# Kernel tuning notes

Measured on AMD Instinct MI355X. Metric: run time of the kernel, lower is better.

## Reference

```python
import jax, jax.numpy as jnp
import numpy as np
import math

B, C, H, W = 32, 256, 64, 64
AUX, RANK, HID, OS = 64, 64, 256, 8


def _fourier(u):
    # u: [B, r] -> take first r//2, sin/cos with freqs linspace(1, pi)
    half = RANK // 2
    w = jnp.linspace(1.0, math.pi, half, dtype=u.dtype)[None, :]
    u = u[:, :half]
    return jnp.concatenate([jnp.sin(u * w), jnp.cos(u * w)], axis=-1)


def setup_inputs() -> dict:
    key = jax.random.key(0)
    ks = jax.random.split(key, 10)

    def lin(k, fan_in, fan_out):
        k1, k2 = jax.random.split(k)
        Wm = jax.random.normal(k1, (fan_in, fan_out), jnp.float32) * 0.02
        bv = jax.random.normal(k2, (fan_out,), jnp.float32) * 0.02
        return Wm, bv

    d = C + AUX
    W_pre, b_pre = lin(ks[0], d, HID)
    W_bc, b_bc = lin(ks[1], HID, C)
    W_bs, b_bs = lin(ks[2], HID, OS)
    W_pc, b_pc = lin(ks[3], HID, RANK)
    W_ps, b_ps = lin(ks[4], HID, RANK)
    W_Wc, b_Wc = lin(ks[5], HID, C * RANK)
    W_Ws, b_Ws = lin(ks[6], HID, OS * RANK)
    x = jax.random.normal(ks[7], (B, C, H, W), jnp.float32)
    a = jax.random.normal(ks[8], (B, AUX), jnp.float32)
    return dict(x=x, a=a, W_pre=W_pre, b_pre=b_pre, W_bc=W_bc, b_bc=b_bc,
                W_bs=W_bs, b_bs=b_bs, W_pc=W_pc, b_pc=b_pc, W_ps=W_ps,
                b_ps=b_ps, W_Wc=W_Wc, b_Wc=b_Wc, W_Ws=W_Ws, b_Ws=b_Ws)


def _m2dm(x, a, W_pre, b_pre, W_bc, b_bc, W_bs, b_bs, W_pc, b_pc,
          W_ps, b_ps, W_Wc, b_Wc, W_Ws, b_Ws):
    Bn, Cn, Hn, Wn = x.shape
    # DynamicProjection
    g = x.mean(axis=(2, 3))                                    # [B,C] GAP
    h = jax.nn.relu(jnp.concatenate([g, a], axis=-1) @ W_pre + b_pre)
    m_base_c = h @ W_bc + b_bc                                 # [B,C]
    m_base_s = h @ W_bs + b_bs                                 # [B,8]
    phi_c = _fourier(h @ W_pc + b_pc)                          # [B,r]
    phi_s = _fourier(h @ W_ps + b_ps)                          # [B,r]
    Wc = (h @ W_Wc + b_Wc).reshape(Bn, Cn, RANK)
    Ws = (h @ W_Ws + b_Ws).reshape(Bn, OS, RANK)
    c_m = m_base_c * jnp.einsum('bcr,br->bc', Wc, phi_c)
    s_m = m_base_s * jnp.einsum('bsr,br->bs', Ws, phi_s)

    # channel modulation
    xc = x * jax.nn.sigmoid(c_m)[:, :, None, None]

    # SpatialModulation: per-sample cross-shaped 3x3 stencil on [avg,max]
    av = x.mean(axis=1)
    mx = x.max(axis=1)
    y = jnp.stack([av, mx], axis=1)                            # [B,2,H,W]
    p = s_m[:, :8].reshape(Bn, 2, 4)                           # up,down,left,right

    def shift(z, di, dj):
        # s[h,w] = z[h+di, w+dj] with zero padding (matches conv2d padding=1)
        zp = jnp.pad(z, ((0, 0), (0, 0), (1, 1), (1, 1)))
        return zp[:, :, 1 + di:1 + di + Hn, 1 + dj:1 + dj + Wn]

    up = shift(y, -1, 0)   # k[0,1] pairs with input row h-1
    dn = shift(y, 1, 0)    # k[2,1]
    lf = shift(y, 0, -1)   # k[1,0]
    rt = shift(y, 0, 1)    # k[1,2]
    pw = p[..., None, None]                                    # [B,2,4,1,1]
    center = -p.sum(axis=-1)[..., None, None]                  # k[1,1] = -sum
    conv = (pw[:, :, 0] * up + pw[:, :, 1] * dn +
            pw[:, :, 2] * lf + pw[:, :, 3] * rt + center * y).sum(axis=1)  # [B,H,W]
    xs = x * jax.nn.sigmoid(conv)[:, None, :, :]
    return x + xc + xs


def reference(x, a, W_pre, b_pre, W_bc, b_bc, W_bs, b_bs, W_pc, b_pc,
              W_ps, b_ps, W_Wc, b_Wc, W_Ws, b_Ws):
    return _m2dm(x, a, W_pre, b_pre, W_bc, b_bc, W_bs, b_bs, W_pc, b_pc,
                 W_ps, b_ps, W_Wc, b_Wc, W_Ws, b_Ws)
```

## Files before the change

### kernel.cpp

```cpp
#include <hip/hip_runtime.h>
#include <math.h>

#define BN   32
#define CN   256
#define HWN  4096
#define AUXN 64
#define RANKN 64
#define HIDN 256
#define OSN  8

#define WS_GPART 0
#define WS_H     131072
#define WS_PHIC  139264
#define WS_MBC   141312
#define WS_SM    149504
#define WS_SIGC  149760
#define WS_Y     157952
#define WS_SIGS  420096

#define TSTR 264

__global__ __launch_bounds__(256) void k_stats(const float* __restrict__ x,
                                               float* __restrict__ gpart,
                                               float* __restrict__ y) {
  int b = blockIdx.y, tile = blockIdx.x, t = threadIdx.x;
  int px = tile * 256 + t;
  const float* xb = x + (size_t)b * CN * HWN;
  __shared__ __align__(16) float tl[64 * TSTR];
  __shared__ float red[256];
  float s = 0.f, m = -INFINITY;
  float* gp = gpart + ((size_t)b * 16 + tile) * 256;
  for (int cc = 0; cc < 4; cc++) {
#pragma unroll 16
    for (int cl = 0; cl < 64; cl++) {
      float v = xb[(size_t)(cc * 64 + cl) * HWN + px];
      s += v;
      m = fmaxf(m, v);
      tl[cl * TSTR + t] = v;
    }
    __syncthreads();
    {
      int cl = t >> 2, pg = t & 3;
      const float4* row = (const float4*)(tl + cl * TSTR + pg * 64);
      float4 acc = {0.f, 0.f, 0.f, 0.f};
#pragma unroll
      for (int j = 0; j < 16; j++) {
        float4 v4 = row[j];
        acc.x += v4.x; acc.y += v4.y; acc.z += v4.z; acc.w += v4.w;
      }
      red[t] = acc.x + acc.y + acc.z + acc.w;
    }
    __syncthreads();
    if (t < 64) gp[cc * 64 + t] = red[t * 4] + red[t * 4 + 1] + red[t * 4 + 2] + red[t * 4 + 3];
    __syncthreads();
  }
  y[(size_t)(b * 2 + 0) * HWN + px] = s * (1.0f / 256.0f);
  y[(size_t)(b * 2 + 1) * HWN + px] = m;
}

__global__ __launch_bounds__(256) void k_head(
    const float* __restrict__ gpart, const float* __restrict__ a,
    const float* __restrict__ W_pre, const float* __restrict__ b_pre,
    const float* __restrict__ W_bc,  const float* __restrict__ b_bc,
    const float* __restrict__ W_bs,  const float* __restrict__ b_bs,
    const float* __restrict__ W_pc,  const float* __restrict__ b_pc,
    const float* __restrict__ W_ps,  const float* __restrict__ b_ps,
    const float* __restrict__ W_Ws,  const float* __restrict__ b_Ws,
    float* __restrict__ h_out, float* __restrict__ phic_out,
    float* __restrict__ mbc_out, float* __restrict__ sm_out) {
  int b = blockIdx.x, t = threadIdx.x;
  __shared__ float in_s[320];
  __shared__ float h_s[256];
  __shared__ float phic_s[64], phis_s[64];
  __shared__ float red[512];
  {
    float gsum = 0.f;
#pragma unroll
    for (int tile = 0; tile < 16; tile++) gsum += gpart[((size_t)b * 16 + tile) * 256 + t];
    in_s[t] = gsum * (1.0f / 4096.0f);
  }
  if (t < 64) in_s[256 + t] = a[b * 64 + t];
  __syncthreads();
  float acc = b_pre[t];
  for (int k = 0; k < 320; k++) acc = fmaf(in_s[k], W_pre[k * 256 + t], acc);
  float h = fmaxf(acc, 0.f);
  h_s[t] = h;
  h_out[b * 256 + t] = h;
  __syncthreads();
  if (t < 64) {
    int j = t & 31;
    const float* Wp = (t < 32) ? W_pc : W_ps;
    const float* bp = (t < 32) ? b_pc : b_ps;
    float u = bp[j];
    for (int k = 0; k < 256; k++) u = fmaf(h_s[k], Wp[k * 64 + j], u);
    float wj = 1.0f + (float)j * (3.14159265358979323846f - 1.0f) / 31.0f;
    float su = sinf(u * wj), cu = cosf(u * wj);
    float* ph = (t < 32) ? phic_s : phis_s;
    ph[j] = su;
    ph[32 + j] = cu;
  }
  __syncthreads();
  if (t < 64) phic_out[b * 64 + t] = phic_s[t];
  float mb = b_bc[t];
  for (int k = 0; k < 256; k++) mb = fmaf(h_s[k], W_bc[k * 256 + t], mb);
  mbc_out[b * 256 + t] = mb;
#pragma unroll
  for (int i = 0; i < 2; i++) {
    int idx = t + 256 * i;
    int s = idx >> 6, r = idx & 63;
    float v = b_Ws[s * 64 + r];
    for (int k = 0; k < 256; k++) v = fmaf(h_s[k], W_Ws[k * 512 + s * 64 + r], v);
    red[idx] = v * phis_s[r];
  }
  __syncthreads();
  if (t < 8) {
    float mbs = b_bs[t];
    for (int k = 0; k < 256; k++) mbs = fmaf(h_s[k], W_bs[k * 8 + t], mbs);
    float sum = 0.f;
    for (int r = 0; r < 64; r++) sum += red[t * 64 + r];
    sm_out[b * 8 + t] = mbs * sum;
  }
}

__global__ __launch_bounds__(512) void k_cm_conv(
    const float* __restrict__ W_Wc, const float* __restrict__ b_Wc,
    const float* __restrict__ h_ws, const float* __restrict__ phic_ws,
    const float* __restrict__ mbc_ws, float* __restrict__ sigc_out,
    const float* __restrict__ y, const float* __restrict__ sm,
    float* __restrict__ sigs) {
  __shared__ __align__(16) float smem[27136];
  int t = threadIdx.x;
  if (blockIdx.x < 256) {
    int c = blockIdx.x;
    float* wsl   = smem;
    float* h_s   = smem + 16384;
    float* phi_s = smem + 24576;
    float* red   = smem + 26624;
    const float* col = W_Wc + (size_t)c * 64;
    for (int i = t; i < 16384; i += 512) {
      int k = i >> 6, r = i & 63;
      wsl[i] = col[(size_t)k * 16384 + r];
    }
    for (int i = t; i < 8192; i += 512) {
      int b = i >> 8, k = i & 255;
      h_s[k * 32 + b] = h_ws[i];
    }
    for (int i = t; i < 2048; i += 512) phi_s[i] = phic_ws[i];
    __syncthreads();
    int b = t >> 4, rq = t & 15;
    float4 q = {0.f, 0.f, 0.f, 0.f};
    const float4* wv = (const float4*)wsl;
    for (int k = 0; k < 256; k++) {
      float4 w4 = wv[k * 16 + rq];
      float hb = h_s[k * 32 + b];
      q.x = fmaf(hb, w4.x, q.x);
      q.y = fmaf(hb, w4.y, q.y);
      q.z = fmaf(hb, w4.z, q.z);
      q.w = fmaf(hb, w4.w, q.w);
    }
    int r0 = rq * 4;
    float4 bw = ((const float4*)(b_Wc + (size_t)c * 64))[rq];
    float part = (q.x + bw.x) * phi_s[b * 64 + r0 + 0] +
                 (q.y + bw.y) * phi_s[b * 64 + r0 + 1] +
                 (q.z + bw.z) * phi_s[b * 64 + r0 + 2] +
                 (q.w + bw.w) * phi_s[b * 64 + r0 + 3];
    red[t] = part;
    __syncthreads();
    if (t < 32) {
      float sum = 0.f;
      for (int i = 0; i < 16; i++) sum += red[t * 16 + i];
      float v = mbc_ws[t * 256 + c] * sum;
      sigc_out[t * 256 + c] = 1.f / (1.f + expf(-v));
    }
  } else {
    int b = blockIdx.x - 256;
    float* ys = smem;
    float* pc = smem + 8192;
    for (int i = t; i < 8192; i += 512) ys[i] = y[b * 8192 + i];
    if (t < 8) pc[t] = sm[b * 8 + t];
    __syncthreads();
    if (t == 0) {
      pc[8] = -(pc[0] + pc[1] + pc[2] + pc[3]);
      pc[9] = -(pc[4] + pc[5] + pc[6] + pc[7]);
    }
    __syncthreads();
    for (int px = t; px < 4096; px += 512) {
      int i = px >> 6, j = px & 63;
      float conv = 0.f;
#pragma unroll
      for (int k = 0; k < 2; k++) {
        const float* yk = ys + k * 4096;
        float up = (i > 0)  ? yk[px - 64] : 0.f;
        float dn = (i < 63) ? yk[px + 64] : 0.f;
        float lf = (j > 0)  ? yk[px - 1]  : 0.f;
        float rt = (j < 63) ? yk[px + 1]  : 0.f;
        conv += pc[k * 4 + 0] * up + pc[k * 4 + 1] * dn + pc[k * 4 + 2] * lf +
                pc[k * 4 + 3] * rt + pc[8 + k] * yk[px];
      }
      sigs[b * 4096 + px] = 1.f / (1.f + expf(-conv));
    }
  }
}

__global__ __launch_bounds__(256) void k_final(const float* __restrict__ x,
                                               const float* __restrict__ sigc,
                                               const float* __restrict__ sigs,
                                               float* __restrict__ out) {
  size_t idx4 = (size_t)blockIdx.x * 256 + threadIdx.x;
  size_t flat = idx4 * 4;
  int b = (int)(flat >> 20);
  int c = (int)((flat >> 12) & 255);
  int px = (int)(flat & 4095);
  float4 xv = ((const float4*)x)[idx4];
  float sc = 1.0f + sigc[b * 256 + c];
  float4 ss = ((const float4*)sigs)[((size_t)b * HWN + px) >> 2];
  float4 o;
  o.x = xv.x * (sc + ss.x);
  o.y = xv.y * (sc + ss.y);
  o.z = xv.z * (sc + ss.z);
  o.w = xv.w * (sc + ss.w);
  ((float4*)out)[idx4] = o;
}

extern "C" void kernel_launch(void* const* d_in, const int* in_sizes, int n_in,
                              void* d_out, int out_size, void* d_ws, size_t ws_size,
                              hipStream_t stream) {
  const float* x     = (const float*)d_in[0];
  const float* a     = (const float*)d_in[1];
  const float* W_pre = (const float*)d_in[2];
  const float* b_pre = (const float*)d_in[3];
  const float* W_bc  = (const float*)d_in[4];
  const float* b_bc  = (const float*)d_in[5];
  const float* W_bs  = (const float*)d_in[6];
  const float* b_bs  = (const float*)d_in[7];
  const float* W_pc  = (const float*)d_in[8];
  const float* b_pc  = (const float*)d_in[9];
  const float* W_ps  = (const float*)d_in[10];
  const float* b_ps  = (const float*)d_in[11];
  const float* W_Wc  = (const float*)d_in[12];
  const float* b_Wc  = (const float*)d_in[13];
  const float* W_Ws  = (const float*)d_in[14];
  const float* b_Ws  = (const float*)d_in[15];
  float* out = (float*)d_out;
  float* ws  = (float*)d_ws;

  float* gpart_ws = ws + WS_GPART;
  float* h_ws     = ws + WS_H;
  float* phic_ws  = ws + WS_PHIC;
  float* mbc_ws   = ws + WS_MBC;
  float* sm_ws    = ws + WS_SM;
  float* sigc_ws  = ws + WS_SIGC;
  float* y_ws     = ws + WS_Y;
  float* sigs_ws  = ws + WS_SIGS;

  k_stats<<<dim3(16, BN), 256, 0, stream>>>(x, gpart_ws, y_ws);
  k_head<<<BN, 256, 0, stream>>>(gpart_ws, a, W_pre, b_pre, W_bc, b_bc, W_bs, b_bs,
                                 W_pc, b_pc, W_ps, b_ps, W_Ws, b_Ws,
                                 h_ws, phic_ws, mbc_ws, sm_ws);
  k_cm_conv<<<CN + BN, 512, 0, stream>>>(W_Wc, b_Wc, h_ws, phic_ws, mbc_ws, sigc_ws,
                                         y_ws, sm_ws, sigs_ws);
  k_final<<<(BN * CN * HWN) / 4 / 256, 256, 0, stream>>>(x, sigc_ws, sigs_ws, out);
}
```

Baseline: 364.5 us.

## Restructure stats reduction, move spatial conv into head, retile channel-modulation GEMV

k_stats now reads x as float4 with each wave covering 64 channels, builds per-channel partial sums through a padded LDS tile, and merges the sum/max across waves. The spatial conv moves from k_cm_conv into k_head, and h is stored transposed so k_cm can copy it with vectorised loads. k_cm is retiled so each thread covers 8 batches with K split across 8 groups and a two-stage reduction, reusing each loaded weight vector 8 times. The head also splits the phi and base-s projections over more threads. The goal is fewer memory passes and better data reuse, at the cost of more LDS use and extra reduction steps.

```diff
diff --git a/kernel.cpp b/kernel.cpp
--- a/kernel.cpp
+++ b/kernel.cpp
@@ -10,7 +10,7 @@
 #define OSN  8
 
 #define WS_GPART 0
-#define WS_H     131072
+#define WS_HT    131072
 #define WS_PHIC  139264
 #define WS_MBC   141312
 #define WS_SM    149504
@@ -18,44 +18,56 @@
 #define WS_Y     157952
 #define WS_SIGS  420096
 
-#define TSTR 264
-
 __global__ __launch_bounds__(256) void k_stats(const float* __restrict__ x,
                                                float* __restrict__ gpart,
                                                float* __restrict__ y) {
   int b = blockIdx.y, tile = blockIdx.x, t = threadIdx.x;
-  int px = tile * 256 + t;
-  const float* xb = x + (size_t)b * CN * HWN;
-  __shared__ __align__(16) float tl[64 * TSTR];
-  __shared__ float red[256];
-  float s = 0.f, m = -INFINITY;
-  float* gp = gpart + ((size_t)b * 16 + tile) * 256;
-  for (int cc = 0; cc < 4; cc++) {
-#pragma unroll 16
-    for (int cl = 0; cl < 64; cl++) {
-      float v = xb[(size_t)(cc * 64 + cl) * HWN + px];
-      s += v;
-      m = fmaxf(m, v);
-      tl[cl * TSTR + t] = v;
+  int w = t >> 6, l = t & 63;
+  __shared__ float csum[256 * 65];
+  __shared__ float4 s_comb[4][64];
+  __shared__ float4 m_comb[4][64];
+  const float4* xb4 = (const float4*)(x + (size_t)b * CN * HWN + tile * 256);
+  float4 s4 = {0.f, 0.f, 0.f, 0.f};
+  float4 m4 = {-INFINITY, -INFINITY, -INFINITY, -INFINITY};
+  int c0 = w << 6;
+#pragma unroll 8
+  for (int cl = 0; cl < 64; cl++) {
+    int c = c0 + cl;
+    float4 v = xb4[(size_t)c * 1024 + l];
+    s4.x += v.x; s4.y += v.y; s4.z += v.z; s4.w += v.w;
+    m4.x = fmaxf(m4.x, v.x); m4.y = fmaxf(m4.y, v.y);
+    m4.z = fmaxf(m4.z, v.z); m4.w = fmaxf(m4.w, v.w);
+    csum[c * 65 + l] = (v.x + v.y) + (v.z + v.w);
+  }
+  s_comb[w][l] = s4;
+  m_comb[w][l] = m4;
+  __syncthreads();
+  {
+    const volatile float* row = csum + t * 65;
+    float g0 = 0.f, g1 = 0.f, g2 = 0.f, g3 = 0.f;
+#pragma unroll
+    for (int j = 0; j < 64; j += 4) {
+      g0 += row[j]; g1 += row[j + 1]; g2 += row[j + 2]; g3 += row[j + 3];
     }
-    __syncthreads();
-    {
-      int cl = t >> 2, pg = t & 3;
-      const float4* row = (const float4*)(tl + cl * TSTR + pg * 64);
-      float4 acc = {0.f, 0.f, 0.f, 0.f};
-#pragma unroll
-      for (int j = 0; j < 16; j++) {
-        float4 v4 = row[j];
-        acc.x += v4.x; acc.y += v4.y; acc.z += v4.z; acc.w += v4.w;
-      }
-      red[t] = acc.x + acc.y + acc.z + acc.w;
-    }
-    __syncthreads();
-    if (t < 64) gp[cc * 64 + t] = red[t * 4] + red[t * 4 + 1] + red[t * 4 + 2] + red[t * 4 + 3];
-    __syncthreads();
-  }
-  y[(size_t)(b * 2 + 0) * HWN + px] = s * (1.0f / 256.0f);
-  y[(size_t)(b * 2 + 1) * HWN + px] = m;
+    gpart[(((size_t)b * 16 + tile) << 8) + t] = (g0 + g1) + (g2 + g3);
+  }
+  if (w == 0) {
+    float4 a0 = s_comb[0][l], a1 = s_comb[1][l], a2 = s_comb[2][l], a3 = s_comb[3][l];
+    float4 b0 = m_comb[0][l], b1 = m_comb[1][l], b2 = m_comb[2][l], b3 = m_comb[3][l];
+    float4 sa, ma;
+    sa.x = (a0.x + a1.x) + (a2.x + a3.x);
+    sa.y = (a0.y + a1.y) + (a2.y + a3.y);
+    sa.z = (a0.z + a1.z) + (a2.z + a3.z);
+    sa.w = (a0.w + a1.w) + (a2.w + a3.w);
+    ma.x = fmaxf(fmaxf(b0.x, b1.x), fmaxf(b2.x, b3.x));
+    ma.y = fmaxf(fmaxf(b0.y, b1.y), fmaxf(b2.y, b3.y));
+    ma.z = fmaxf(fmaxf(b0.z, b1.z), fmaxf(b2.z, b3.z));
+    ma.w = fmaxf(fmaxf(b0.w, b1.w), fmaxf(b2.w, b3.w));
+    const float inv = 1.0f / 256.0f;
+    float4 avg = {sa.x * inv, sa.y * inv, sa.z * inv, sa.w * inv};
+    ((float4*)(y + (size_t)b * 2 * HWN + tile * 256))[l] = avg;
+    ((float4*)(y + ((size_t)b * 2 + 1) * HWN + tile * 256))[l] = ma;
+  }
 }
 
 __global__ __launch_bounds__(256) void k_head(
@@ -66,17 +78,21 @@
     const float* __restrict__ W_pc,  const float* __restrict__ b_pc,
     const float* __restrict__ W_ps,  const float* __restrict__ b_ps,
     const float* __restrict__ W_Ws,  const float* __restrict__ b_Ws,
-    float* __restrict__ h_out, float* __restrict__ phic_out,
-    float* __restrict__ mbc_out, float* __restrict__ sm_out) {
+    const float* __restrict__ y,
+    float* __restrict__ h_t_out, float* __restrict__ phic_out,
+    float* __restrict__ mbc_out, float* __restrict__ sigs) {
   int b = blockIdx.x, t = threadIdx.x;
   __shared__ float in_s[320];
   __shared__ float h_s[256];
   __shared__ float phic_s[64], phis_s[64];
   __shared__ float red[512];
+  __shared__ float red2[256];
+  __shared__ float pc[10];
   {
     float gsum = 0.f;
 #pragma unroll
-    for (int tile = 0; tile < 16; tile++) gsum += gpart[((size_t)b * 16 + tile) * 256 + t];
+    for (int tile = 0; tile < 16; tile++)
+      gsum += gpart[(((size_t)b * 16 + tile) << 8) + t];
     in_s[t] = gsum * (1.0f / 4096.0f);
   }
   if (t < 64) in_s[256 + t] = a[b * 64 + t];
@@ -85,14 +101,21 @@
   for (int k = 0; k < 320; k++) acc = fmaf(in_s[k], W_pre[k * 256 + t], acc);
   float h = fmaxf(acc, 0.f);
   h_s[t] = h;
-  h_out[b * 256 + t] = h;
+  h_t_out[t * 32 + b] = h;
+  __syncthreads();
+  {
+    int ui = t & 63, kg = t >> 6, j = ui & 31;
+    const float* Wp = (ui < 32) ? W_pc : W_ps;
+    float u = 0.f;
+    int k0 = kg << 6;
+    for (int k = k0; k < k0 + 64; k++) u = fmaf(h_s[k], Wp[k * 64 + j], u);
+    red2[(ui << 2) | kg] = u;
+  }
   __syncthreads();
   if (t < 64) {
     int j = t & 31;
-    const float* Wp = (t < 32) ? W_pc : W_ps;
     const float* bp = (t < 32) ? b_pc : b_ps;
-    float u = bp[j];
-    for (int k = 0; k < 256; k++) u = fmaf(h_s[k], Wp[k * 64 + j], u);
+    float u = bp[j] + (red2[t * 4] + red2[t * 4 + 1]) + (red2[t * 4 + 2] + red2[t * 4 + 3]);
     float wj = 1.0f + (float)j * (3.14159265358979323846f - 1.0f) / 31.0f;
     float su = sinf(u * wj), cu = cosf(u * wj);
     float* ph = (t < 32) ? phic_s : phis_s;
@@ -112,93 +135,118 @@
     for (int k = 0; k < 256; k++) v = fmaf(h_s[k], W_Ws[k * 512 + s * 64 + r], v);
     red[idx] = v * phis_s[r];
   }
+  {
+    int s = t & 7, kg = t >> 3;
+    float v = 0.f;
+    int k0 = kg << 3;
+#pragma unroll
+    for (int k = k0; k < k0 + 8; k++) v = fmaf(h_s[k], W_bs[k * 8 + s], v);
+    red2[t] = v;
+  }
   __syncthreads();
   if (t < 8) {
     float mbs = b_bs[t];
-    for (int k = 0; k < 256; k++) mbs = fmaf(h_s[k], W_bs[k * 8 + t], mbs);
+#pragma unroll
+    for (int kg = 0; kg < 32; kg++) mbs += red2[kg * 8 + t];
     float sum = 0.f;
     for (int r = 0; r < 64; r++) sum += red[t * 64 + r];
-    sm_out[b * 8 + t] = mbs * sum;
-  }
-}
-
-__global__ __launch_bounds__(512) void k_cm_conv(
+    pc[t] = mbs * sum;
+  }
+  __syncthreads();
+  if (t == 0) {
+    pc[8] = -(pc[0] + pc[1] + pc[2] + pc[3]);
+    pc[9] = -(pc[4] + pc[5] + pc[6] + pc[7]);
+  }
+  __syncthreads();
+  const float* yb = y + (size_t)b * 2 * HWN;
+  for (int px = t; px < 4096; px += 256) {
+    int i = px >> 6, j = px & 63;
+    float conv = 0.f;
+#pragma unroll
+    for (int k = 0; k < 2; k++) {
+      const float* yk = yb + k * 4096;
+      float up = (i > 0)  ? yk[px - 64] : 0.f;
+      float dn = (i < 63) ? yk[px + 64] : 0.f;
+      float lf = (j > 0)  ? yk[px - 1]  : 0.f;
+      float rt = (j < 63) ? yk[px + 1]  : 0.f;
+      conv += pc[k * 4 + 0] * up + pc[k * 4 + 1] * dn + pc[k * 4 + 2] * lf +
+              pc[k * 4 + 3] * rt + pc[8 + k] * yk[px];
+    }
+    sigs[b * 4096 + px] = 1.f / (1.f + expf(-conv));
+  }
+}
+
+__global__ __launch_bounds__(512) void k_cm(
     const float* __restrict__ W_Wc, const float* __restrict__ b_Wc,
-    const float* __restrict__ h_ws, const float* __restrict__ phic_ws,
-    const float* __restrict__ mbc_ws, float* __restrict__ sigc_out,
-    const float* __restrict__ y, const float* __restrict__ sm,
-    float* __restrict__ sigs) {
-  __shared__ __align__(16) float smem[27136];
-  int t = threadIdx.x;
-  if (blockIdx.x < 256) {
-    int c = blockIdx.x;
-    float* wsl   = smem;
-    float* h_s   = smem + 16384;
-    float* phi_s = smem + 24576;
-    float* red   = smem + 26624;
-    const float* col = W_Wc + (size_t)c * 64;
-    for (int i = t; i < 16384; i += 512) {
-      int k = i >> 6, r = i & 63;
-      wsl[i] = col[(size_t)k * 16384 + r];
+    const float* __restrict__ h_t, const float* __restrict__ phic_ws,
+    const float* __restrict__ mbc_ws, float* __restrict__ sigc_out) {
+  __shared__ __align__(16) float wsl[16384];
+  __shared__ __align__(16) float h_s[8192];
+  __shared__ __align__(16) float phi_s[2048];
+  __shared__ float red[4096];
+  __shared__ float red2[512];
+  int t = threadIdx.x, c = blockIdx.x;
+  {
+    const float4* col4 = (const float4*)(W_Wc + (size_t)c * 64);
+    float4* wsl4 = (float4*)wsl;
+#pragma unroll
+    for (int i4 = t; i4 < 4096; i4 += 512) {
+      int k = i4 >> 4, rq = i4 & 15;
+      wsl4[i4] = col4[(size_t)k * 4096 + rq];
     }
-    for (int i = t; i < 8192; i += 512) {
-      int b = i >> 8, k = i & 255;
-      h_s[k * 32 + b] = h_ws[i];
+    const float4* ht4 = (const float4*)h_t;
+    float4* hs4 = (float4*)h_s;
+#pragma unroll
+    for (int i4 = t; i4 < 2048; i4 += 512) hs4[i4] = ht4[i4];
+    ((float4*)phi_s)[t] = ((const float4*)phic_ws)[t];
+  }
+  __syncthreads();
+  int rq = t & 15, b8 = (t >> 4) & 3, kg = t >> 6;
+  const float4* wv = (const float4*)wsl;
+  float4 acc[8];
+#pragma unroll
+  for (int i = 0; i < 8; i++) acc[i] = {0.f, 0.f, 0.f, 0.f};
+#pragma unroll 4
+  for (int kk = 0; kk < 32; kk++) {
+    int k = (kg << 5) + kk;
+    float4 w4 = wv[k * 16 + rq];
+    const float4* hp = (const float4*)(h_s + k * 32 + (b8 << 3));
+    float4 h0 = hp[0], h1 = hp[1];
+    float hv[8] = {h0.x, h0.y, h0.z, h0.w, h1.x, h1.y, h1.z, h1.w};
+#pragma unroll
+    for (int i = 0; i < 8; i++) {
+      acc[i].x = fmaf(hv[i], w4.x, acc[i].x);
+      acc[i].y = fmaf(hv[i], w4.y, acc[i].y);
+      acc[i].z = fmaf(hv[i], w4.z, acc[i].z);
+      acc[i].w = fmaf(hv[i], w4.w, acc[i].w);
     }
-    for (int i = t; i < 2048; i += 512) phi_s[i] = phic_ws[i];
-    __syncthreads();
-    int b = t >> 4, rq = t & 15;
-    float4 q = {0.f, 0.f, 0.f, 0.f};
-    const float4* wv = (const float4*)wsl;
-    for (int k = 0; k < 256; k++) {
-      float4 w4 = wv[k * 16 + rq];
-      float hb = h_s[k * 32 + b];
-      q.x = fmaf(hb, w4.x, q.x);
-      q.y = fmaf(hb, w4.y, q.y);
-      q.z = fmaf(hb, w4.z, q.z);
-      q.w = fmaf(hb, w4.w, q.w);
-    }
-    int r0 = rq * 4;
-    float4 bw = ((const float4*)(b_Wc + (size_t)c * 64))[rq];
-    float part = (q.x + bw.x) * phi_s[b * 64 + r0 + 0] +
-                 (q.y + bw.y) * phi_s[b * 64 + r0 + 1] +
-                 (q.z + bw.z) * phi_s[b * 64 + r0 + 2] +
-                 (q.w + bw.w) * phi_s[b * 64 + r0 + 3];
-    red[t] = part;
-    __syncthreads();
-    if (t < 32) {
-      float sum = 0.f;
-      for (int i = 0; i < 16; i++) sum += red[t * 16 + i];
-      float v = mbc_ws[t * 256 + c] * sum;
-      sigc_out[t * 256 + c] = 1.f / (1.f + expf(-v));
-    }
-  } else {
-    int b = blockIdx.x - 256;
-    float* ys = smem;
-    float* pc = smem + 8192;
-    for (int i = t; i < 8192; i += 512) ys[i] = y[b * 8192 + i];
-    if (t < 8) pc[t] = sm[b * 8 + t];
-    __syncthreads();
-    if (t == 0) {
-      pc[8] = -(pc[0] + pc[1] + pc[2] + pc[3]);
-      pc[9] = -(pc[4] + pc[5] + pc[6] + pc[7]);
-    }
-    __syncthreads();
-    for (int px = t; px < 4096; px += 512) {
-      int i = px >> 6, j = px & 63;
-      float conv = 0.f;
-#pragma unroll
-      for (int k = 0; k < 2; k++) {
-        const float* yk = ys + k * 4096;
-        float up = (i > 0)  ? yk[px - 64] : 0.f;
-        float dn = (i < 63) ? yk[px + 64] : 0.f;
-        float lf = (j > 0)  ? yk[px - 1]  : 0.f;
-        float rt = (j < 63) ? yk[px + 1]  : 0.f;
-        conv += pc[k * 4 + 0] * up + pc[k * 4 + 1] * dn + pc[k * 4 + 2] * lf +
-                pc[k * 4 + 3] * rt + pc[8 + k] * yk[px];
-      }
-      sigs[b * 4096 + px] = 1.f / (1.f + expf(-conv));
-    }
+  }
+  float4 bw = {0.f, 0.f, 0.f, 0.f};
+  if (kg == 0) bw = ((const float4*)(b_Wc + (size_t)c * 64))[rq];
+#pragma unroll
+  for (int i = 0; i < 8; i++) {
+    int bb = (b8 << 3) + i;
+    float4 ph = ((const float4*)phi_s)[bb * 16 + rq];
+    float4 av = acc[i];
+    av.x += bw.x; av.y += bw.y; av.z += bw.z; av.w += bw.w;
+    red[(kg * 32 + bb) * 16 + rq] =
+        (av.x * ph.x + av.y * ph.y) + (av.z * ph.z + av.w * ph.w);
+  }
+  __syncthreads();
+  {
+    int bb = t >> 4, rr = t & 15;
+    float tot = 0.f;
+#pragma unroll
+    for (int g = 0; g < 8; g++) tot += red[(g * 32 + bb) * 16 + rr];
+    red2[t] = tot;
+  }
+  __syncthreads();
+  if (t < 32) {
+    float sum = 0.f;
+#pragma unroll
+    for (int i = 0; i < 16; i++) sum += red2[t * 16 + i];
+    float v = mbc_ws[t * 256 + c] * sum;
+    sigc_out[t * 256 + c] = 1.f / (1.f + expf(-v));
   }
 }
 
@@ -245,19 +293,17 @@
   float* ws  = (float*)d_ws;
 
   float* gpart_ws = ws + WS_GPART;
-  float* h_ws     = ws + WS_H;
+  float* ht_ws    = ws + WS_HT;
   float* phic_ws  = ws + WS_PHIC;
   float* mbc_ws   = ws + WS_MBC;
-  float* sm_ws    = ws + WS_SM;
   float* sigc_ws  = ws + WS_SIGC;
   float* y_ws     = ws + WS_Y;
   float* sigs_ws  = ws + WS_SIGS;
 
   k_stats<<<dim3(16, BN), 256, 0, stream>>>(x, gpart_ws, y_ws);
   k_head<<<BN, 256, 0, stream>>>(gpart_ws, a, W_pre, b_pre, W_bc, b_bc, W_bs, b_bs,
-                                 W_pc, b_pc, W_ps, b_ps, W_Ws, b_Ws,
-                                 h_ws, phic_ws, mbc_ws, sm_ws);
-  k_cm_conv<<<CN + BN, 512, 0, stream>>>(W_Wc, b_Wc, h_ws, phic_ws, mbc_ws, sigc_ws,
-                                         y_ws, sm_ws, sigs_ws);
+                                 W_pc, b_pc, W_ps, b_ps, W_Ws, b_Ws, y_ws,
+                                 ht_ws, phic_ws, mbc_ws, sigs_ws);
+  k_cm<<<CN, 512, 0, stream>>>(W_Wc, b_Wc, ht_ws, phic_ws, mbc_ws, sigc_ws);
   k_final<<<(BN * CN * HWN) / 4 / 256, 256, 0, stream>>>(x, sigc_ws, sigs_ws, out);
 }
```

Result: faster. 343.3 us (-5.8%).
